# Kernel tuning notes

Measured on AMD Instinct MI355X. Metric: run time of the kernel, lower is better.

## Reference

```python
import jax, jax.numpy as jnp
import numpy as np

COST_CLASS = 1.0
COST_BBOX = 1.0
COST_GIOU = 1.0
NUM_TGT_PER_IMG = 100  # sizes[b] for every image (equal-size, padded-batch style)


def box_cxcywh_to_xyxy(b):
    cx, cy, w, h = jnp.split(b, 4, axis=-1)
    return jnp.concatenate([cx - 0.5 * w, cy - 0.5 * h, cx + 0.5 * w, cy + 0.5 * h], axis=-1)


def generalized_box_iou(b1, b2):
    # b1: [N,4], b2: [M,4] in xyxy -> [N,M]
    area1 = (b1[:, 2] - b1[:, 0]) * (b1[:, 3] - b1[:, 1])
    area2 = (b2[:, 2] - b2[:, 0]) * (b2[:, 3] - b2[:, 1])
    lt = jnp.maximum(b1[:, None, :2], b2[None, :, :2])
    rb = jnp.minimum(b1[:, None, 2:], b2[None, :, 2:])
    wh = jnp.clip(rb - lt, 0.0)
    inter = wh[..., 0] * wh[..., 1]
    union = area1[:, None] + area2[None, :] - inter
    iou = inter / union
    lt_e = jnp.minimum(b1[:, None, :2], b2[None, :, :2])
    rb_e = jnp.maximum(b1[:, None, 2:], b2[None, :, 2:])
    wh_e = jnp.clip(rb_e - lt_e, 0.0)
    area_e = wh_e[..., 0] * wh_e[..., 1]
    return iou - (area_e - union) / area_e


def build_cost_matrix(logits, pred_boxes, tgt_labels, tgt_boxes):
    B, Q, C = logits.shape
    out_prob = jax.nn.sigmoid(logits).reshape(B * Q, C)        # [BQ, C]
    out_bbox = pred_boxes.reshape(B * Q, 4)                     # [BQ, 4]
    tgt_ids = tgt_labels.reshape(-1)                            # [BT]
    tgt_bbox = tgt_boxes.reshape(-1, 4)                         # [BT, 4]
    cost_class = -out_prob[:, tgt_ids]                          # [BQ, BT]
    cost_bbox = jnp.sum(jnp.abs(out_bbox[:, None, :] - tgt_bbox[None, :, :]), axis=-1)  # L1 cdist
    cost_giou = -generalized_box_iou(box_cxcywh_to_xyxy(out_bbox), box_cxcywh_to_xyxy(tgt_bbox))
    cost = COST_BBOX * cost_bbox + COST_CLASS * cost_class + COST_GIOU * cost_giou
    return cost.reshape(B, Q, -1)                               # [B, Q, B*T]


def greedy_match(cost, curr_targets):
    # Faithful to _greedy_matcher: iteratively pick the globally smallest-cost
    # unmatched (row, col) pair among columns < curr_targets. Equivalent to the
    # stable-sorted flat scan (argmin breaks ties at lowest flat index, matching
    # the stable ascending sort).
    Q, Ttot = cost.shape
    col_ok = jnp.arange(Ttot) < curr_targets
    c0 = jnp.where(col_ok[None, :], cost, jnp.inf)
    num_match = min(Q, curr_targets)

    def step(c, _):
        idx = jnp.argmin(c.reshape(-1))
        r = idx // Ttot
        col = idx % Ttot
        c = c.at[r, :].set(jnp.inf).at[:, col].set(jnp.inf)
        return c, (r.astype(jnp.int32), col.astype(jnp.int32))

    _, (rows, cols) = jax.lax.scan(step, c0, None, length=num_match)
    return rows, cols


def setup_inputs() -> dict:
    key = jax.random.key(0)
    k1, k2, k3, k4, k5, k6 = jax.random.split(key, 6)
    B, Q, C, T = 16, 900, 91, NUM_TGT_PER_IMG
    logits = jax.random.normal(k1, (B, Q, C), dtype=jnp.float32)
    pb_cxcy = jax.random.uniform(k2, (B, Q, 2), dtype=jnp.float32)
    pb_wh = jax.random.uniform(k3, (B, Q, 2), dtype=jnp.float32, minval=0.05, maxval=0.5)
    pred_boxes = jnp.concatenate([pb_cxcy, pb_wh], axis=-1)
    tgt_labels = jax.random.randint(k4, (B, T), 0, C)
    tb_cxcy = jax.random.uniform(k5, (B, T, 2), dtype=jnp.float32)
    tb_wh = jax.random.uniform(k6, (B, T, 2), dtype=jnp.float32, minval=0.05, maxval=0.5)
    tgt_boxes = jnp.concatenate([tb_cxcy, tb_wh], axis=-1)
    return {"logits": logits, "pred_boxes": pred_boxes, "tgt_labels": tgt_labels, "tgt_boxes": tgt_boxes}


def reference(logits, pred_boxes, tgt_labels, tgt_boxes):
    cost = build_cost_matrix(logits, pred_boxes, tgt_labels, tgt_boxes)  # [B, Q, B*T]
    rows, cols = jax.vmap(lambda c: greedy_match(c, NUM_TGT_PER_IMG))(cost)
    return cost, rows, cols
```

## Files before the change

kernel.cpp:

```cpp
#include <hip/hip_runtime.h>
#include <math.h>

#define BB 16
#define QQ 900
#define CC 91
#define TT 100
#define BT (BB * TT)
#define NTHREADS 256
#define TILE 15
#define NBLK_PER_IMG (QQ / TILE)
#define NSLOT 15
#define WSCOLS 128
#define PENDK 8

__device__ __forceinline__ unsigned ordkey(float f) {
    unsigned u = __float_as_uint(f);
    return (u & 0x80000000u) ? ~u : (u | 0x80000000u);
}

__device__ __forceinline__ unsigned long long u64min(unsigned long long a, unsigned long long b) {
    return a < b ? a : b;
}
__device__ __forceinline__ unsigned long long u64max(unsigned long long a, unsigned long long b) {
    return a > b ? a : b;
}

__device__ __forceinline__ unsigned long long packkrc(unsigned key, int row, int col) {
    return ((unsigned long long)key << 21) | ((unsigned long long)row << 11) | (unsigned)col;
}

__device__ __forceinline__ unsigned long long rdlane64(unsigned long long v, int l) {
    unsigned lo = (unsigned)__builtin_amdgcn_readlane((int)(unsigned)v, l);
    unsigned hi = (unsigned)__builtin_amdgcn_readlane((int)(unsigned)(v >> 32), l);
    return ((unsigned long long)hi << 32) | lo;
}

__global__ __launch_bounds__(NTHREADS) void cost_kernel(
    const float* __restrict__ logits,
    const float* __restrict__ pred,
    const int*   __restrict__ tlab,
    const float* __restrict__ tbox,
    float*       __restrict__ cost,
    unsigned long long* __restrict__ colmin)
{
    const int b  = blockIdx.x / NBLK_PER_IMG;
    const int tb = blockIdx.x % NBLK_PER_IMG;
    const int r0 = tb * TILE;

    __shared__ float4 s_t[BT];
    __shared__ int    s_lab[BT];
    __shared__ float  s_sig[TILE][CC];
    __shared__ float  s_row[TILE][8];

    for (int j = threadIdx.x; j < BT; j += NTHREADS) {
        s_t[j] = *(const float4*)(tbox + (size_t)j * 4);
        s_lab[j] = tlab[j];
    }
    for (int u = threadIdx.x; u < TILE * CC; u += NTHREADS) {
        int r = u / CC, c = u % CC;
        float x = logits[((size_t)(b * QQ + r0 + r)) * CC + c];
        s_sig[r][c] = 1.0f / (1.0f + expf(-x));
    }
    if (threadIdx.x < TILE) {
        int r = threadIdx.x;
        const float4 p = *(const float4*)(pred + ((size_t)(b * QQ + r0 + r)) * 4);
        s_row[r][0] = p.x; s_row[r][1] = p.y; s_row[r][2] = p.z; s_row[r][3] = p.w;
        s_row[r][4] = p.x - 0.5f * p.z;
        s_row[r][5] = p.y - 0.5f * p.w;
        s_row[r][6] = p.x + 0.5f * p.z;
        s_row[r][7] = p.y + 0.5f * p.w;
    }
    __syncthreads();

    unsigned long long bestc = ~0ULL;

    for (int r = 0; r < TILE; ++r) {
        const float px  = s_row[r][0], py  = s_row[r][1], pz  = s_row[r][2], pw  = s_row[r][3];
        const float p_x0 = s_row[r][4], p_y0 = s_row[r][5], p_x1 = s_row[r][6], p_y1 = s_row[r][7];
        const float area1 = (p_x1 - p_x0) * (p_y1 - p_y0);
        float* crow = cost + ((size_t)(b * QQ + r0 + r)) * BT;

        for (int j = threadIdx.x; j < BT; j += NTHREADS) {
            float4 t = s_t[j];
            float cclass = -s_sig[r][s_lab[j]];
            float cbbox = ((fabsf(px - t.x) + fabsf(py - t.y)) + fabsf(pz - t.z)) + fabsf(pw - t.w);

            float t_x0 = t.x - 0.5f * t.z, t_y0 = t.y - 0.5f * t.w;
            float t_x1 = t.x + 0.5f * t.z, t_y1 = t.y + 0.5f * t.w;
            float area2 = (t_x1 - t_x0) * (t_y1 - t_y0);

            float ltx = fmaxf(p_x0, t_x0), lty = fmaxf(p_y0, t_y0);
            float rbx = fminf(p_x1, t_x1), rby = fminf(p_y1, t_y1);
            float iw = fmaxf(rbx - ltx, 0.0f), ih = fmaxf(rby - lty, 0.0f);
            float inter = iw * ih;
            float uni = (area1 + area2) - inter;
            float iou = inter / uni;

            float ex0 = fminf(p_x0, t_x0), ey0 = fminf(p_y0, t_y0);
            float ex1 = fmaxf(p_x1, t_x1), ey1 = fmaxf(p_y1, t_y1);
            float ew = fmaxf(ex1 - ex0, 0.0f), eh = fmaxf(ey1 - ey0, 0.0f);
            float ae = ew * eh;
            float giou = iou - (ae - uni) / ae;

            float v = (cbbox + cclass) + (-giou);
            __builtin_nontemporal_store(v, &crow[j]);
            if (j < TT) bestc = u64min(bestc, packkrc(ordkey(v), r0 + r, j));
        }
    }

    if (threadIdx.x < TT)
        atomicMin(colmin + (size_t)b * WSCOLS + threadIdx.x, bestc);
}

__global__ __launch_bounds__(64, 1) void greedy_kernel(
    const float* __restrict__ cost,
    const unsigned long long* __restrict__ colmin,
    float*       __restrict__ rows_out,
    float*       __restrict__ cols_out)
{
    const int b = blockIdx.x;
    const int lane = threadIdx.x;
    const float* cb = cost + (size_t)b * QQ * BT;

    __shared__ unsigned s_first[1024];
    __shared__ unsigned s_dead32[256];
    unsigned char* s_dead = (unsigned char*)s_dead32;

    #pragma unroll
    for (int kk = 0; kk < 4; ++kk) s_dead32[lane + kk * 64] = 0u;

    unsigned long long va = colmin[(size_t)b * WSCOLS + lane];
    unsigned long long vb = (lane < TT - 64)
                          ? colmin[(size_t)b * WSCOLS + 64 + lane] : ~0ULL;

    #pragma unroll
    for (int k = 2; k <= 128; k <<= 1) {
        #pragma unroll
        for (int j = k >> 1; j > 0; j >>= 1) {
            if (j == 64) {
                unsigned long long lo = u64min(va, vb);
                unsigned long long hi = va ^ vb ^ lo;
                va = lo; vb = hi;
            } else {
                unsigned long long pa = __shfl_xor(va, j, 64);
                bool ta = ((lane & j) == 0) == ((lane & k) == 0);
                va = ta ? u64min(va, pa) : u64max(va, pa);
                unsigned long long pb = __shfl_xor(vb, j, 64);
                int ib = lane + 64;
                bool tb_ = ((ib & j) == 0) == ((ib & k) == 0);
                vb = tb_ ? u64min(vb, pb) : u64max(vb, pb);
            }
        }
    }

    const int rA = (int)((va >> 11) & 0x3FF);
    const int cA = (int)(va & 0x7FF);
    const int rB = (int)((vb >> 11) & 0x3FF);
    const int cB = (int)(vb & 0x7FF);

    unsigned long long pend[PENDK];
    #pragma unroll
    for (int t = 0; t < PENDK; ++t) pend[t] = ~0ULL;
    unsigned long long pmin = ~0ULL;

    int cur = 0;
    int m = 0;

    while (m < TT) {
        __asm__ volatile("s_waitcnt lgkmcnt(0)" ::: "memory");

        #pragma unroll
        for (int kk = 0; kk < 16; ++kk) s_first[lane + kk * 64] = 0xFFFFFFFFu;

        bool dA = s_dead[rA] != 0;
        bool dB = s_dead[rB] != 0;
        __asm__ volatile("s_waitcnt lgkmcnt(0)" ::: "memory");

        bool inA = (lane >= cur) && !dA;
        bool inB = ((64 + lane) >= cur) && !dB;
        if (inA) atomicMin(&s_first[rA], (unsigned)lane);
        if (inB) atomicMin(&s_first[rB], (unsigned)(64 + lane));
        __asm__ volatile("s_waitcnt lgkmcnt(0)" ::: "memory");

        bool dupA = inA && (s_first[rA] < (unsigned)lane);
        bool dupB = inB && (s_first[rB] < (unsigned)(64 + lane));

        bool evA = (lane >= cur)        && (dA || dupA || (pmin < va));
        bool evB = ((64 + lane) >= cur) && (dB || dupB || (pmin < vb));
        unsigned long long mA = __ballot(evA);
        unsigned long long mB = __ballot(evB);
        int k = mA ? (int)__ffsll(mA) - 1
              : (mB ? 64 + (int)__ffsll(mB) - 1 : 128);

        int n = k - cur;
        if (n > TT - m) n = TT - m;

        if (n > 0) {
            int iA = lane - cur;
            if (iA >= 0 && iA < n) {
                rows_out[b * TT + m + iA] = (float)rA;
                cols_out[b * TT + m + iA] = (float)cA;
                s_dead[rA] = 1;
            }
            int iB = 64 + lane - cur;
            if (iB >= 0 && iB < n) {
                rows_out[b * TT + m + iB] = (float)rB;
                cols_out[b * TT + m + iB] = (float)cB;
                s_dead[rB] = 1;
            }
            m += n;
            cur += n;
            if (m >= TT) break;
        }

        unsigned long long ecur = (cur < 64) ? rdlane64(va, cur)
                                : (cur < 128) ? rdlane64(vb, cur - 64) : ~0ULL;
        __asm__ volatile("s_waitcnt lgkmcnt(0)" ::: "memory");

        if (pmin < ecur) {
            unsigned long long e = pmin;
            bool removed = false;
            #pragma unroll
            for (int t = 0; t < PENDK; ++t)
                if (!removed && pend[t] == e) { pend[t] = ~0ULL; removed = true; }
            pmin = ~0ULL;
            #pragma unroll
            for (int t = 0; t < PENDK; ++t) pmin = u64min(pmin, pend[t]);

            int re = (int)((e >> 11) & 0x3FF);
            int ce = (int)(e & 0x7FF);
            bool alive = (s_dead[re] == 0);
            if (alive) {
                if (lane == 0) {
                    rows_out[b * TT + m] = (float)re;
                    cols_out[b * TT + m] = (float)ce;
                    s_dead[re] = 1;
                }
                ++m;
            } else {
                unsigned long long best = ~0ULL;
                #pragma unroll
                for (int i = 0; i < NSLOT; ++i) {
                    int r = i * 64 + lane;
                    bool ok = (r < QQ) && (s_dead[r] == 0);
                    if (ok) {
                        float v = cb[(size_t)r * BT + ce];
                        best = u64min(best, packkrc(ordkey(v), r, ce));
                    }
                }
                #pragma unroll
                for (int off = 1; off < 64; off <<= 1)
                    best = u64min(best, __shfl_xor(best, off, 64));
                bool placed = false;
                #pragma unroll
                for (int t = 0; t < PENDK; ++t)
                    if (!placed && pend[t] == ~0ULL) { pend[t] = best; placed = true; }
                pmin = u64min(pmin, best);
            }
        } else {
            int cc = (int)(ecur & 0x7FF);
            unsigned long long best = ~0ULL;
            #pragma unroll
            for (int i = 0; i < NSLOT; ++i) {
                int r = i * 64 + lane;
                bool ok = (r < QQ) && (s_dead[r] == 0);
                if (ok) {
                    float v = cb[(size_t)r * BT + cc];
                    best = u64min(best, packkrc(ordkey(v), r, cc));
                }
            }
            #pragma unroll
            for (int off = 1; off < 64; off <<= 1)
                best = u64min(best, __shfl_xor(best, off, 64));
            bool placed = false;
            #pragma unroll
            for (int t = 0; t < PENDK; ++t)
                if (!placed && pend[t] == ~0ULL) { pend[t] = best; placed = true; }
            pmin = u64min(pmin, best);
            ++cur;
        }
    }
}

extern "C" void kernel_launch(void* const* d_in, const int* in_sizes, int n_in,
                              void* d_out, int out_size, void* d_ws, size_t ws_size,
                              hipStream_t stream) {
    const float* logits = (const float*)d_in[0];
    const float* pred   = (const float*)d_in[1];
    const int*   tlab   = (const int*)d_in[2];
    const float* tbox   = (const float*)d_in[3];

    float* out = (float*)d_out;
    float* cost = out;
    float* rows = out + (size_t)BB * QQ * BT;
    float* cols = rows + (size_t)BB * TT;

    unsigned long long* colmin = (unsigned long long*)d_ws;

    hipMemsetAsync(d_ws, 0xFF, (size_t)BB * WSCOLS * sizeof(unsigned long long), stream);

    cost_kernel<<<BB * NBLK_PER_IMG, NTHREADS, 0, stream>>>(logits, pred, tlab, tbox, cost, colmin);
    greedy_kernel<<<BB, 64, 0, stream>>>(cost, colmin, rows, cols);
}
```

Baseline: 217.4 us.

## Fuse cost and greedy kernels with per-image completion counters

Merges the cost-matrix and greedy-matching kernels into one launch. Greedy blocks are appended after the cost blocks and spin on a per-image done counter (decremented atomically by each cost block) before starting. The per-image greedy work can then begin as soon as that image's rows finish, removing a kernel boundary. The change also register-blocks five rows per target in the cost loop, replaces nontemporal stores with plain stores, and precomputes the duplicate-row detection once instead of on every iteration. The risks are deadlock if the greedy blocks are scheduled before the cost blocks they wait on, and a loop guard that could cut matching short.

```diff
diff --git a/kernel.cpp b/kernel.cpp
--- a/kernel.cpp
+++ b/kernel.cpp
@@ -9,129 +9,179 @@
 #define NTHREADS 256
 #define TILE 15
 #define NBLK_PER_IMG (QQ / TILE)
+#define COST_BLOCKS (BB * NBLK_PER_IMG)
 #define NSLOT 15
 #define WSCOLS 128
 #define PENDK 8
+#define RB 5
+#define DONE_TGT 0xFFFFFFC3u
 
 __device__ __forceinline__ unsigned ordkey(float f) {
     unsigned u = __float_as_uint(f);
     return (u & 0x80000000u) ? ~u : (u | 0x80000000u);
 }
-
 __device__ __forceinline__ unsigned long long u64min(unsigned long long a, unsigned long long b) {
     return a < b ? a : b;
 }
 __device__ __forceinline__ unsigned long long u64max(unsigned long long a, unsigned long long b) {
     return a > b ? a : b;
 }
-
 __device__ __forceinline__ unsigned long long packkrc(unsigned key, int row, int col) {
     return ((unsigned long long)key << 21) | ((unsigned long long)row << 11) | (unsigned)col;
 }
-
 __device__ __forceinline__ unsigned long long rdlane64(unsigned long long v, int l) {
     unsigned lo = (unsigned)__builtin_amdgcn_readlane((int)(unsigned)v, l);
     unsigned hi = (unsigned)__builtin_amdgcn_readlane((int)(unsigned)(v >> 32), l);
     return ((unsigned long long)hi << 32) | lo;
 }
 
-__global__ __launch_bounds__(NTHREADS) void cost_kernel(
+__device__ __forceinline__ unsigned long long rescan_col(
+    const float* __restrict__ cb, const unsigned char* s_dead, int cc, int lane)
+{
+    unsigned long long best = ~0ULL;
+    #pragma unroll
+    for (int i = 0; i < NSLOT; ++i) {
+        int r = i * 64 + lane;
+        if (r < QQ && s_dead[r] == 0) {
+            float v = __hip_atomic_load(cb + (size_t)r * BT + cc,
+                                        __ATOMIC_RELAXED, __HIP_MEMORY_SCOPE_AGENT);
+            best = u64min(best, packkrc(ordkey(v), r, cc));
+        }
+    }
+    #pragma unroll
+    for (int off = 1; off < 64; off <<= 1)
+        best = u64min(best, __shfl_xor(best, off, 64));
+    return best;
+}
+
+struct SmCost {
+    float4 t[BT];
+    int    lab[BT];
+    float  sig[TILE][CC];
+    float  row[TILE][8];
+};
+struct SmGreedy {
+    unsigned fr[1024];
+    unsigned dead32[256];
+};
+union SmAll { SmCost c; SmGreedy g; };
+
+__global__ __launch_bounds__(NTHREADS, 4) void fused_kernel(
     const float* __restrict__ logits,
     const float* __restrict__ pred,
     const int*   __restrict__ tlab,
     const float* __restrict__ tbox,
     float*       __restrict__ cost,
-    unsigned long long* __restrict__ colmin)
-{
-    const int b  = blockIdx.x / NBLK_PER_IMG;
-    const int tb = blockIdx.x % NBLK_PER_IMG;
-    const int r0 = tb * TILE;
-
-    __shared__ float4 s_t[BT];
-    __shared__ int    s_lab[BT];
-    __shared__ float  s_sig[TILE][CC];
-    __shared__ float  s_row[TILE][8];
-
-    for (int j = threadIdx.x; j < BT; j += NTHREADS) {
-        s_t[j] = *(const float4*)(tbox + (size_t)j * 4);
-        s_lab[j] = tlab[j];
-    }
-    for (int u = threadIdx.x; u < TILE * CC; u += NTHREADS) {
-        int r = u / CC, c = u % CC;
-        float x = logits[((size_t)(b * QQ + r0 + r)) * CC + c];
-        s_sig[r][c] = 1.0f / (1.0f + expf(-x));
-    }
-    if (threadIdx.x < TILE) {
-        int r = threadIdx.x;
-        const float4 p = *(const float4*)(pred + ((size_t)(b * QQ + r0 + r)) * 4);
-        s_row[r][0] = p.x; s_row[r][1] = p.y; s_row[r][2] = p.z; s_row[r][3] = p.w;
-        s_row[r][4] = p.x - 0.5f * p.z;
-        s_row[r][5] = p.y - 0.5f * p.w;
-        s_row[r][6] = p.x + 0.5f * p.z;
-        s_row[r][7] = p.y + 0.5f * p.w;
-    }
-    __syncthreads();
-
-    unsigned long long bestc = ~0ULL;
-
-    for (int r = 0; r < TILE; ++r) {
-        const float px  = s_row[r][0], py  = s_row[r][1], pz  = s_row[r][2], pw  = s_row[r][3];
-        const float p_x0 = s_row[r][4], p_y0 = s_row[r][5], p_x1 = s_row[r][6], p_y1 = s_row[r][7];
-        const float area1 = (p_x1 - p_x0) * (p_y1 - p_y0);
-        float* crow = cost + ((size_t)(b * QQ + r0 + r)) * BT;
-
-        for (int j = threadIdx.x; j < BT; j += NTHREADS) {
-            float4 t = s_t[j];
-            float cclass = -s_sig[r][s_lab[j]];
-            float cbbox = ((fabsf(px - t.x) + fabsf(py - t.y)) + fabsf(pz - t.z)) + fabsf(pw - t.w);
-
-            float t_x0 = t.x - 0.5f * t.z, t_y0 = t.y - 0.5f * t.w;
-            float t_x1 = t.x + 0.5f * t.z, t_y1 = t.y + 0.5f * t.w;
-            float area2 = (t_x1 - t_x0) * (t_y1 - t_y0);
-
-            float ltx = fmaxf(p_x0, t_x0), lty = fmaxf(p_y0, t_y0);
-            float rbx = fminf(p_x1, t_x1), rby = fminf(p_y1, t_y1);
-            float iw = fmaxf(rbx - ltx, 0.0f), ih = fmaxf(rby - lty, 0.0f);
-            float inter = iw * ih;
-            float uni = (area1 + area2) - inter;
-            float iou = inter / uni;
-
-            float ex0 = fminf(p_x0, t_x0), ey0 = fminf(p_y0, t_y0);
-            float ex1 = fmaxf(p_x1, t_x1), ey1 = fmaxf(p_y1, t_y1);
-            float ew = fmaxf(ex1 - ex0, 0.0f), eh = fmaxf(ey1 - ey0, 0.0f);
-            float ae = ew * eh;
-            float giou = iou - (ae - uni) / ae;
-
-            float v = (cbbox + cclass) + (-giou);
-            __builtin_nontemporal_store(v, &crow[j]);
-            if (j < TT) bestc = u64min(bestc, packkrc(ordkey(v), r0 + r, j));
-        }
-    }
-
-    if (threadIdx.x < TT)
-        atomicMin(colmin + (size_t)b * WSCOLS + threadIdx.x, bestc);
-}
-
-__global__ __launch_bounds__(64, 1) void greedy_kernel(
-    const float* __restrict__ cost,
-    const unsigned long long* __restrict__ colmin,
+    unsigned long long* __restrict__ colmin,
+    unsigned*    __restrict__ done,
     float*       __restrict__ rows_out,
     float*       __restrict__ cols_out)
 {
-    const int b = blockIdx.x;
+    __shared__ SmAll sm;
+
+    if (blockIdx.x < COST_BLOCKS) {
+        const int b  = blockIdx.x / NBLK_PER_IMG;
+        const int tb = blockIdx.x % NBLK_PER_IMG;
+        const int r0 = tb * TILE;
+
+        for (int j = threadIdx.x; j < BT; j += NTHREADS) {
+            sm.c.t[j]   = *(const float4*)(tbox + (size_t)j * 4);
+            sm.c.lab[j] = tlab[j];
+        }
+        for (int u = threadIdx.x; u < TILE * CC; u += NTHREADS) {
+            int r = u / CC, c = u % CC;
+            float x = logits[((size_t)(b * QQ + r0 + r)) * CC + c];
+            sm.c.sig[r][c] = 1.0f / (1.0f + expf(-x));
+        }
+        if (threadIdx.x < TILE) {
+            int r = threadIdx.x;
+            const float4 p = *(const float4*)(pred + ((size_t)(b * QQ + r0 + r)) * 4);
+            sm.c.row[r][0] = p.x; sm.c.row[r][1] = p.y;
+            sm.c.row[r][2] = p.z; sm.c.row[r][3] = p.w;
+            sm.c.row[r][4] = p.x - 0.5f * p.z;
+            sm.c.row[r][5] = p.y - 0.5f * p.w;
+            sm.c.row[r][6] = p.x + 0.5f * p.z;
+            sm.c.row[r][7] = p.y + 0.5f * p.w;
+        }
+        __syncthreads();
+
+        unsigned long long bestc = ~0ULL;
+
+        for (int p0 = 0; p0 < TILE; p0 += RB) {
+            float qx[RB], qy[RB], qz[RB], qw[RB];
+            float qx0[RB], qy0[RB], qx1[RB], qy1[RB], qa1[RB];
+            #pragma unroll
+            for (int rr = 0; rr < RB; ++rr) {
+                const int r = p0 + rr;
+                qx[rr]  = sm.c.row[r][0]; qy[rr]  = sm.c.row[r][1];
+                qz[rr]  = sm.c.row[r][2]; qw[rr]  = sm.c.row[r][3];
+                qx0[rr] = sm.c.row[r][4]; qy0[rr] = sm.c.row[r][5];
+                qx1[rr] = sm.c.row[r][6]; qy1[rr] = sm.c.row[r][7];
+                qa1[rr] = (qx1[rr] - qx0[rr]) * (qy1[rr] - qy0[rr]);
+            }
+            for (int j = threadIdx.x; j < BT; j += NTHREADS) {
+                float4 t = sm.c.t[j];
+                int id = sm.c.lab[j];
+                float t_x0 = t.x - 0.5f * t.z, t_y0 = t.y - 0.5f * t.w;
+                float t_x1 = t.x + 0.5f * t.z, t_y1 = t.y + 0.5f * t.w;
+                float area2 = (t_x1 - t_x0) * (t_y1 - t_y0);
+                #pragma unroll
+                for (int rr = 0; rr < RB; ++rr) {
+                    float cclass = -sm.c.sig[p0 + rr][id];
+                    float cbbox = ((fabsf(qx[rr] - t.x) + fabsf(qy[rr] - t.y))
+                                 + fabsf(qz[rr] - t.z)) + fabsf(qw[rr] - t.w);
+
+                    float ltx = fmaxf(qx0[rr], t_x0), lty = fmaxf(qy0[rr], t_y0);
+                    float rbx = fminf(qx1[rr], t_x1), rby = fminf(qy1[rr], t_y1);
+                    float iw = fmaxf(rbx - ltx, 0.0f), ih = fmaxf(rby - lty, 0.0f);
+                    float inter = iw * ih;
+                    float uni = (qa1[rr] + area2) - inter;
+                    float iou = inter / uni;
+
+                    float ex0 = fminf(qx0[rr], t_x0), ey0 = fminf(qy0[rr], t_y0);
+                    float ex1 = fmaxf(qx1[rr], t_x1), ey1 = fmaxf(qy1[rr], t_y1);
+                    float ew = fmaxf(ex1 - ex0, 0.0f), eh = fmaxf(ey1 - ey0, 0.0f);
+                    float ae = ew * eh;
+                    float giou = iou - (ae - uni) / ae;
+
+                    float v = (cbbox + cclass) + (-giou);
+                    cost[((size_t)(b * QQ + r0 + p0 + rr)) * BT + j] = v;
+                    if (j < TT)
+                        bestc = u64min(bestc, packkrc(ordkey(v), r0 + p0 + rr, j));
+                }
+            }
+        }
+
+        if (threadIdx.x < TT)
+            atomicMin(colmin + (size_t)b * WSCOLS + threadIdx.x, bestc);
+        __threadfence();
+        __syncthreads();
+        if (threadIdx.x == 0)
+            atomicSub(done + b, 1u);
+        return;
+    }
+
+    const int b = blockIdx.x - COST_BLOCKS;
+    if (threadIdx.x >= 64) return;
     const int lane = threadIdx.x;
     const float* cb = cost + (size_t)b * QQ * BT;
-
-    __shared__ unsigned s_first[1024];
-    __shared__ unsigned s_dead32[256];
-    unsigned char* s_dead = (unsigned char*)s_dead32;
-
-    #pragma unroll
-    for (int kk = 0; kk < 4; ++kk) s_dead32[lane + kk * 64] = 0u;
-
-    unsigned long long va = colmin[(size_t)b * WSCOLS + lane];
+    unsigned char* s_dead = (unsigned char*)sm.g.dead32;
+
+    #pragma unroll
+    for (int k = 0; k < 16; ++k) sm.g.fr[lane + 64 * k] = 0xFFFFFFFFu;
+    #pragma unroll
+    for (int k = 0; k < 4; ++k) sm.g.dead32[lane + 64 * k] = 0u;
+
+    while (__hip_atomic_load(done + b, __ATOMIC_ACQUIRE, __HIP_MEMORY_SCOPE_AGENT) != DONE_TGT)
+        __builtin_amdgcn_s_sleep(2);
+    __threadfence();
+
+    unsigned long long va = __hip_atomic_load(colmin + (size_t)b * WSCOLS + lane,
+                                              __ATOMIC_RELAXED, __HIP_MEMORY_SCOPE_AGENT);
     unsigned long long vb = (lane < TT - 64)
-                          ? colmin[(size_t)b * WSCOLS + 64 + lane] : ~0ULL;
+        ? __hip_atomic_load(colmin + (size_t)b * WSCOLS + 64 + lane,
+                            __ATOMIC_RELAXED, __HIP_MEMORY_SCOPE_AGENT)
+        : ~0ULL;
 
     #pragma unroll
     for (int k = 2; k <= 128; k <<= 1) {
@@ -158,35 +208,28 @@
     const int rB = (int)((vb >> 11) & 0x3FF);
     const int cB = (int)(vb & 0x7FF);
 
+    atomicMin(&sm.g.fr[rA], (unsigned)lane);
+    atomicMin(&sm.g.fr[rB], (unsigned)(64 + lane));
+    __threadfence_block();
+    unsigned frA = sm.g.fr[rA], frB = sm.g.fr[rB];
+    const unsigned fdA = (frA < (unsigned)lane)       ? frA : 0xFFFFFFFFu;
+    const unsigned fdB = (frB < (unsigned)(64 + lane)) ? frB : 0xFFFFFFFFu;
+
     unsigned long long pend[PENDK];
     #pragma unroll
     for (int t = 0; t < PENDK; ++t) pend[t] = ~0ULL;
     unsigned long long pmin = ~0ULL;
 
-    int cur = 0;
-    int m = 0;
-
-    while (m < TT) {
-        __asm__ volatile("s_waitcnt lgkmcnt(0)" ::: "memory");
-
-        #pragma unroll
-        for (int kk = 0; kk < 16; ++kk) s_first[lane + kk * 64] = 0xFFFFFFFFu;
-
+    int cur = 0, m = 0, guard = 0;
+    while (m < TT && ++guard < 4096) {
+        __threadfence_block();
         bool dA = s_dead[rA] != 0;
         bool dB = s_dead[rB] != 0;
-        __asm__ volatile("s_waitcnt lgkmcnt(0)" ::: "memory");
-
-        bool inA = (lane >= cur) && !dA;
-        bool inB = ((64 + lane) >= cur) && !dB;
-        if (inA) atomicMin(&s_first[rA], (unsigned)lane);
-        if (inB) atomicMin(&s_first[rB], (unsigned)(64 + lane));
-        __asm__ volatile("s_waitcnt lgkmcnt(0)" ::: "memory");
-
-        bool dupA = inA && (s_first[rA] < (unsigned)lane);
-        bool dupB = inB && (s_first[rB] < (unsigned)(64 + lane));
-
-        bool evA = (lane >= cur)        && (dA || dupA || (pmin < va));
-        bool evB = ((64 + lane) >= cur) && (dB || dupB || (pmin < vb));
+
+        bool evA = (lane >= cur) &&
+                   (dA || (fdA != 0xFFFFFFFFu && fdA >= (unsigned)cur) || (pmin < va));
+        bool evB = ((64 + lane) >= cur) &&
+                   (dB || (fdB != 0xFFFFFFFFu && fdB >= (unsigned)cur) || (pmin < vb));
         unsigned long long mA = __ballot(evA);
         unsigned long long mB = __ballot(evB);
         int k = mA ? (int)__ffsll(mA) - 1
@@ -194,7 +237,6 @@
 
         int n = k - cur;
         if (n > TT - m) n = TT - m;
-
         if (n > 0) {
             int iA = lane - cur;
             if (iA >= 0 && iA < n) {
@@ -208,14 +250,13 @@
                 cols_out[b * TT + m + iB] = (float)cB;
                 s_dead[rB] = 1;
             }
-            m += n;
-            cur += n;
+            m += n; cur += n;
             if (m >= TT) break;
         }
 
         unsigned long long ecur = (cur < 64) ? rdlane64(va, cur)
                                 : (cur < 128) ? rdlane64(vb, cur - 64) : ~0ULL;
-        __asm__ volatile("s_waitcnt lgkmcnt(0)" ::: "memory");
+        __threadfence_block();
 
         if (pmin < ecur) {
             unsigned long long e = pmin;
@@ -238,40 +279,16 @@
                 }
                 ++m;
             } else {
-                unsigned long long best = ~0ULL;
-                #pragma unroll
-                for (int i = 0; i < NSLOT; ++i) {
-                    int r = i * 64 + lane;
-                    bool ok = (r < QQ) && (s_dead[r] == 0);
-                    if (ok) {
-                        float v = cb[(size_t)r * BT + ce];
-                        best = u64min(best, packkrc(ordkey(v), r, ce));
-                    }
-                }
-                #pragma unroll
-                for (int off = 1; off < 64; off <<= 1)
-                    best = u64min(best, __shfl_xor(best, off, 64));
+                unsigned long long best = rescan_col(cb, s_dead, ce, lane);
                 bool placed = false;
                 #pragma unroll
                 for (int t = 0; t < PENDK; ++t)
                     if (!placed && pend[t] == ~0ULL) { pend[t] = best; placed = true; }
                 pmin = u64min(pmin, best);
             }
-        } else {
-            int cc = (int)(ecur & 0x7FF);
-            unsigned long long best = ~0ULL;
-            #pragma unroll
-            for (int i = 0; i < NSLOT; ++i) {
-                int r = i * 64 + lane;
-                bool ok = (r < QQ) && (s_dead[r] == 0);
-                if (ok) {
-                    float v = cb[(size_t)r * BT + cc];
-                    best = u64min(best, packkrc(ordkey(v), r, cc));
-                }
-            }
-            #pragma unroll
-            for (int off = 1; off < 64; off <<= 1)
-                best = u64min(best, __shfl_xor(best, off, 64));
+        } else if (cur < 128) {
+            int ccur = (int)(ecur & 0x7FF);
+            unsigned long long best = rescan_col(cb, s_dead, ccur, lane);
             bool placed = false;
             #pragma unroll
             for (int t = 0; t < PENDK; ++t)
@@ -296,9 +313,10 @@
     float* cols = rows + (size_t)BB * TT;
 
     unsigned long long* colmin = (unsigned long long*)d_ws;
-
-    hipMemsetAsync(d_ws, 0xFF, (size_t)BB * WSCOLS * sizeof(unsigned long long), stream);
-
-    cost_kernel<<<BB * NBLK_PER_IMG, NTHREADS, 0, stream>>>(logits, pred, tlab, tbox, cost, colmin);
-    greedy_kernel<<<BB, 64, 0, stream>>>(cost, colmin, rows, cols);
-}
+    unsigned* done = (unsigned*)((char*)d_ws + (size_t)BB * WSCOLS * 8);
+
+    hipMemsetAsync(d_ws, 0xFF, (size_t)BB * WSCOLS * 8 + (size_t)BB * 4, stream);
+
+    fused_kernel<<<COST_BLOCKS + BB, NTHREADS, 0, stream>>>(
+        logits, pred, tlab, tbox, cost, colmin, done, rows, cols);
+}
```

After: 285.1 us. +31.1%, slower.

## Replace atomic column-min with per-block slots, register-block rows, hoist duplicate detection

Applied to the files above, without the earlier changes.

The cost kernel now processes five query rows per target load, keeping the row box values in registers, and uses plain stores instead of nontemporal stores. Instead of a memset plus global atomicMin, each block writes its per-column minimum into its own workspace slot, and the greedy kernel reduces the 60 slots per image itself. Duplicate-row detection in the greedy loop is computed once up front rather than re-initialising 1024 shared words and issuing atomics every iteration, and an iteration guard is added. In exchange there is more workspace traffic and a serial slot reduction at the start of the single-wave greedy kernel, and dropping the nontemporal hint may change cache behaviour.

```diff
diff --git a/kernel.cpp b/kernel.cpp
--- a/kernel.cpp
+++ b/kernel.cpp
@@ -9,26 +9,25 @@
 #define NTHREADS 256
 #define TILE 15
 #define NBLK_PER_IMG (QQ / TILE)
+#define COST_BLOCKS (BB * NBLK_PER_IMG)
 #define NSLOT 15
-#define WSCOLS 128
 #define PENDK 8
+#define RB 5
+#define SLOT_STRIDE 100
 
 __device__ __forceinline__ unsigned ordkey(float f) {
     unsigned u = __float_as_uint(f);
     return (u & 0x80000000u) ? ~u : (u | 0x80000000u);
 }
-
 __device__ __forceinline__ unsigned long long u64min(unsigned long long a, unsigned long long b) {
     return a < b ? a : b;
 }
 __device__ __forceinline__ unsigned long long u64max(unsigned long long a, unsigned long long b) {
     return a > b ? a : b;
 }
-
 __device__ __forceinline__ unsigned long long packkrc(unsigned key, int row, int col) {
     return ((unsigned long long)key << 21) | ((unsigned long long)row << 11) | (unsigned)col;
 }
-
 __device__ __forceinline__ unsigned long long rdlane64(unsigned long long v, int l) {
     unsigned lo = (unsigned)__builtin_amdgcn_readlane((int)(unsigned)v, l);
     unsigned hi = (unsigned)__builtin_amdgcn_readlane((int)(unsigned)(v >> 32), l);
@@ -41,7 +40,7 @@
     const int*   __restrict__ tlab,
     const float* __restrict__ tbox,
     float*       __restrict__ cost,
-    unsigned long long* __restrict__ colmin)
+    unsigned long long* __restrict__ slots)
 {
     const int b  = blockIdx.x / NBLK_PER_IMG;
     const int tb = blockIdx.x % NBLK_PER_IMG;
@@ -53,7 +52,7 @@
     __shared__ float  s_row[TILE][8];
 
     for (int j = threadIdx.x; j < BT; j += NTHREADS) {
-        s_t[j] = *(const float4*)(tbox + (size_t)j * 4);
+        s_t[j]   = *(const float4*)(tbox + (size_t)j * 4);
         s_lab[j] = tlab[j];
     }
     for (int u = threadIdx.x; u < TILE * CC; u += NTHREADS) {
@@ -64,7 +63,8 @@
     if (threadIdx.x < TILE) {
         int r = threadIdx.x;
         const float4 p = *(const float4*)(pred + ((size_t)(b * QQ + r0 + r)) * 4);
-        s_row[r][0] = p.x; s_row[r][1] = p.y; s_row[r][2] = p.z; s_row[r][3] = p.w;
+        s_row[r][0] = p.x; s_row[r][1] = p.y;
+        s_row[r][2] = p.z; s_row[r][3] = p.w;
         s_row[r][4] = p.x - 0.5f * p.z;
         s_row[r][5] = p.y - 0.5f * p.w;
         s_row[r][6] = p.x + 0.5f * p.z;
@@ -74,47 +74,58 @@
 
     unsigned long long bestc = ~0ULL;
 
-    for (int r = 0; r < TILE; ++r) {
-        const float px  = s_row[r][0], py  = s_row[r][1], pz  = s_row[r][2], pw  = s_row[r][3];
-        const float p_x0 = s_row[r][4], p_y0 = s_row[r][5], p_x1 = s_row[r][6], p_y1 = s_row[r][7];
-        const float area1 = (p_x1 - p_x0) * (p_y1 - p_y0);
-        float* crow = cost + ((size_t)(b * QQ + r0 + r)) * BT;
-
+    for (int p0 = 0; p0 < TILE; p0 += RB) {
+        float qx[RB], qy[RB], qz[RB], qw[RB];
+        float qx0[RB], qy0[RB], qx1[RB], qy1[RB], qa1[RB];
+        #pragma unroll
+        for (int rr = 0; rr < RB; ++rr) {
+            const int r = p0 + rr;
+            qx[rr]  = s_row[r][0]; qy[rr]  = s_row[r][1];
+            qz[rr]  = s_row[r][2]; qw[rr]  = s_row[r][3];
+            qx0[rr] = s_row[r][4]; qy0[rr] = s_row[r][5];
+            qx1[rr] = s_row[r][6]; qy1[rr] = s_row[r][7];
+            qa1[rr] = (qx1[rr] - qx0[rr]) * (qy1[rr] - qy0[rr]);
+        }
         for (int j = threadIdx.x; j < BT; j += NTHREADS) {
             float4 t = s_t[j];
-            float cclass = -s_sig[r][s_lab[j]];
-            float cbbox = ((fabsf(px - t.x) + fabsf(py - t.y)) + fabsf(pz - t.z)) + fabsf(pw - t.w);
-
+            int id = s_lab[j];
             float t_x0 = t.x - 0.5f * t.z, t_y0 = t.y - 0.5f * t.w;
             float t_x1 = t.x + 0.5f * t.z, t_y1 = t.y + 0.5f * t.w;
             float area2 = (t_x1 - t_x0) * (t_y1 - t_y0);
-
-            float ltx = fmaxf(p_x0, t_x0), lty = fmaxf(p_y0, t_y0);
-            float rbx = fminf(p_x1, t_x1), rby = fminf(p_y1, t_y1);
-            float iw = fmaxf(rbx - ltx, 0.0f), ih = fmaxf(rby - lty, 0.0f);
-            float inter = iw * ih;
-            float uni = (area1 + area2) - inter;
-            float iou = inter / uni;
-
-            float ex0 = fminf(p_x0, t_x0), ey0 = fminf(p_y0, t_y0);
-            float ex1 = fmaxf(p_x1, t_x1), ey1 = fmaxf(p_y1, t_y1);
-            float ew = fmaxf(ex1 - ex0, 0.0f), eh = fmaxf(ey1 - ey0, 0.0f);
-            float ae = ew * eh;
-            float giou = iou - (ae - uni) / ae;
-
-            float v = (cbbox + cclass) + (-giou);
-            __builtin_nontemporal_store(v, &crow[j]);
-            if (j < TT) bestc = u64min(bestc, packkrc(ordkey(v), r0 + r, j));
+            #pragma unroll
+            for (int rr = 0; rr < RB; ++rr) {
+                float cclass = -s_sig[p0 + rr][id];
+                float cbbox = ((fabsf(qx[rr] - t.x) + fabsf(qy[rr] - t.y))
+                             + fabsf(qz[rr] - t.z)) + fabsf(qw[rr] - t.w);
+
+                float ltx = fmaxf(qx0[rr], t_x0), lty = fmaxf(qy0[rr], t_y0);
+                float rbx = fminf(qx1[rr], t_x1), rby = fminf(qy1[rr], t_y1);
+                float iw = fmaxf(rbx - ltx, 0.0f), ih = fmaxf(rby - lty, 0.0f);
+                float inter = iw * ih;
+                float uni = (qa1[rr] + area2) - inter;
+                float iou = inter / uni;
+
+                float ex0 = fminf(qx0[rr], t_x0), ey0 = fminf(qy0[rr], t_y0);
+                float ex1 = fmaxf(qx1[rr], t_x1), ey1 = fmaxf(qy1[rr], t_y1);
+                float ew = fmaxf(ex1 - ex0, 0.0f), eh = fmaxf(ey1 - ey0, 0.0f);
+                float ae = ew * eh;
+                float giou = iou - (ae - uni) / ae;
+
+                float v = (cbbox + cclass) + (-giou);
+                cost[((size_t)(b * QQ + r0 + p0 + rr)) * BT + j] = v;
+                if (j < TT)
+                    bestc = u64min(bestc, packkrc(ordkey(v), r0 + p0 + rr, j));
+            }
         }
     }
 
     if (threadIdx.x < TT)
-        atomicMin(colmin + (size_t)b * WSCOLS + threadIdx.x, bestc);
+        slots[((size_t)(b * NBLK_PER_IMG) + tb) * SLOT_STRIDE + threadIdx.x] = bestc;
 }
 
 __global__ __launch_bounds__(64, 1) void greedy_kernel(
     const float* __restrict__ cost,
-    const unsigned long long* __restrict__ colmin,
+    const unsigned long long* __restrict__ slots,
     float*       __restrict__ rows_out,
     float*       __restrict__ cols_out)
 {
@@ -122,16 +133,23 @@
     const int lane = threadIdx.x;
     const float* cb = cost + (size_t)b * QQ * BT;
 
-    __shared__ unsigned s_first[1024];
+    __shared__ unsigned s_fr[1024];
     __shared__ unsigned s_dead32[256];
     unsigned char* s_dead = (unsigned char*)s_dead32;
 
     #pragma unroll
-    for (int kk = 0; kk < 4; ++kk) s_dead32[lane + kk * 64] = 0u;
-
-    unsigned long long va = colmin[(size_t)b * WSCOLS + lane];
-    unsigned long long vb = (lane < TT - 64)
-                          ? colmin[(size_t)b * WSCOLS + 64 + lane] : ~0ULL;
+    for (int k = 0; k < 16; ++k) s_fr[lane + 64 * k] = 0xFFFFFFFFu;
+    #pragma unroll
+    for (int k = 0; k < 4; ++k) s_dead32[lane + 64 * k] = 0u;
+
+    const unsigned long long* sb = slots + (size_t)b * NBLK_PER_IMG * SLOT_STRIDE;
+    unsigned long long va = ~0ULL, vb = ~0ULL;
+    #pragma unroll 10
+    for (int t = 0; t < NBLK_PER_IMG; ++t) {
+        va = u64min(va, sb[(size_t)t * SLOT_STRIDE + lane]);
+        if (lane < TT - 64)
+            vb = u64min(vb, sb[(size_t)t * SLOT_STRIDE + 64 + lane]);
+    }
 
     #pragma unroll
     for (int k = 2; k <= 128; k <<= 1) {
@@ -158,35 +176,28 @@
     const int rB = (int)((vb >> 11) & 0x3FF);
     const int cB = (int)(vb & 0x7FF);
 
+    atomicMin(&s_fr[rA], (unsigned)lane);
+    atomicMin(&s_fr[rB], (unsigned)(64 + lane));
+    __threadfence_block();
+    unsigned frA = s_fr[rA], frB = s_fr[rB];
+    const unsigned fdA = (frA < (unsigned)lane)        ? frA : 0xFFFFFFFFu;
+    const unsigned fdB = (frB < (unsigned)(64 + lane)) ? frB : 0xFFFFFFFFu;
+
     unsigned long long pend[PENDK];
     #pragma unroll
     for (int t = 0; t < PENDK; ++t) pend[t] = ~0ULL;
     unsigned long long pmin = ~0ULL;
 
-    int cur = 0;
-    int m = 0;
-
-    while (m < TT) {
-        __asm__ volatile("s_waitcnt lgkmcnt(0)" ::: "memory");
-
-        #pragma unroll
-        for (int kk = 0; kk < 16; ++kk) s_first[lane + kk * 64] = 0xFFFFFFFFu;
-
+    int cur = 0, m = 0, guard = 0;
+    while (m < TT && ++guard < 2048) {
+        __threadfence_block();
         bool dA = s_dead[rA] != 0;
         bool dB = s_dead[rB] != 0;
-        __asm__ volatile("s_waitcnt lgkmcnt(0)" ::: "memory");
-
-        bool inA = (lane >= cur) && !dA;
-        bool inB = ((64 + lane) >= cur) && !dB;
-        if (inA) atomicMin(&s_first[rA], (unsigned)lane);
-        if (inB) atomicMin(&s_first[rB], (unsigned)(64 + lane));
-        __asm__ volatile("s_waitcnt lgkmcnt(0)" ::: "memory");
-
-        bool dupA = inA && (s_first[rA] < (unsigned)lane);
-        bool dupB = inB && (s_first[rB] < (unsigned)(64 + lane));
-
-        bool evA = (lane >= cur)        && (dA || dupA || (pmin < va));
-        bool evB = ((64 + lane) >= cur) && (dB || dupB || (pmin < vb));
+
+        bool evA = (lane >= cur) &&
+                   (dA || (fdA != 0xFFFFFFFFu && fdA >= (unsigned)cur) || (pmin < va));
+        bool evB = ((64 + lane) >= cur) &&
+                   (dB || (fdB != 0xFFFFFFFFu && fdB >= (unsigned)cur) || (pmin < vb));
         unsigned long long mA = __ballot(evA);
         unsigned long long mB = __ballot(evB);
         int k = mA ? (int)__ffsll(mA) - 1
@@ -194,7 +205,6 @@
 
         int n = k - cur;
         if (n > TT - m) n = TT - m;
-
         if (n > 0) {
             int iA = lane - cur;
             if (iA >= 0 && iA < n) {
@@ -208,14 +218,13 @@
                 cols_out[b * TT + m + iB] = (float)cB;
                 s_dead[rB] = 1;
             }
-            m += n;
-            cur += n;
+            m += n; cur += n;
             if (m >= TT) break;
         }
 
         unsigned long long ecur = (cur < 64) ? rdlane64(va, cur)
                                 : (cur < 128) ? rdlane64(vb, cur - 64) : ~0ULL;
-        __asm__ volatile("s_waitcnt lgkmcnt(0)" ::: "memory");
+        __threadfence_block();
 
         if (pmin < ecur) {
             unsigned long long e = pmin;
@@ -242,8 +251,7 @@
                 #pragma unroll
                 for (int i = 0; i < NSLOT; ++i) {
                     int r = i * 64 + lane;
-                    bool ok = (r < QQ) && (s_dead[r] == 0);
-                    if (ok) {
+                    if (r < QQ && s_dead[r] == 0) {
                         float v = cb[(size_t)r * BT + ce];
                         best = u64min(best, packkrc(ordkey(v), r, ce));
                     }
@@ -257,16 +265,15 @@
                     if (!placed && pend[t] == ~0ULL) { pend[t] = best; placed = true; }
                 pmin = u64min(pmin, best);
             }
-        } else {
-            int cc = (int)(ecur & 0x7FF);
+        } else if (cur < 128) {
+            int ccur = (int)(ecur & 0x7FF);
             unsigned long long best = ~0ULL;
             #pragma unroll
             for (int i = 0; i < NSLOT; ++i) {
                 int r = i * 64 + lane;
-                bool ok = (r < QQ) && (s_dead[r] == 0);
-                if (ok) {
-                    float v = cb[(size_t)r * BT + cc];
-                    best = u64min(best, packkrc(ordkey(v), r, cc));
+                if (r < QQ && s_dead[r] == 0) {
+                    float v = cb[(size_t)r * BT + ccur];
+                    best = u64min(best, packkrc(ordkey(v), r, ccur));
                 }
             }
             #pragma unroll
@@ -295,10 +302,8 @@
     float* rows = out + (size_t)BB * QQ * BT;
     float* cols = rows + (size_t)BB * TT;
 
-    unsigned long long* colmin = (unsigned long long*)d_ws;
-
-    hipMemsetAsync(d_ws, 0xFF, (size_t)BB * WSCOLS * sizeof(unsigned long long), stream);
-
-    cost_kernel<<<BB * NBLK_PER_IMG, NTHREADS, 0, stream>>>(logits, pred, tlab, tbox, cost, colmin);
-    greedy_kernel<<<BB, 64, 0, stream>>>(cost, colmin, rows, cols);
-}
+    unsigned long long* slots = (unsigned long long*)d_ws;
+
+    cost_kernel<<<COST_BLOCKS, NTHREADS, 0, stream>>>(logits, pred, tlab, tbox, cost, slots);
+    greedy_kernel<<<BB, 64, 0, stream>>>(cost, slots, rows, cols);
+}
```

New measurement: 204.0 us. 6.2% less time.
